# Performance work log

Measured on AMD Instinct MI355X. Metric: run time of the kernel, lower is better.

## Reference

```python
import jax, jax.numpy as jnp
import numpy as np

VEC_DIM = 128
N_DOCS = 100000
N_WORDS = 100000
B = 16384
CTX = 8
NS = 16


def setup_inputs() -> dict:
    key = jax.random.key(0)
    k1, k2, k3, k4, k5 = jax.random.split(key, 5)
    doc_ids = jax.random.randint(k1, (B,), 0, N_DOCS)
    context_ids = jax.random.randint(k2, (B, CTX), 0, N_WORDS)
    sample_ids = jax.random.randint(k3, (B, NS), 0, N_WORDS)
    paragraph_matrix = jax.random.normal(k4, (N_DOCS, VEC_DIM), dtype=jnp.float32)
    word_matrix = jax.random.normal(k5, (N_WORDS, VEC_DIM), dtype=jnp.float32)
    outputs = jnp.zeros((VEC_DIM, N_WORDS), dtype=jnp.float32)
    return {
        "doc_ids": doc_ids,
        "context_ids": context_ids,
        "sample_ids": sample_ids,
        "paragraph_matrix": paragraph_matrix,
        "word_matrix": word_matrix,
        "outputs": outputs,
    }


def reference(doc_ids, context_ids, sample_ids, paragraph_matrix, word_matrix, outputs):
    # inputs: [B, D] = doc embedding + sum of context word embeddings
    inputs = paragraph_matrix[doc_ids] + jnp.sum(word_matrix[context_ids], axis=1)
    # sampled output columns: [B, D, NS]
    out_cols = outputs[:, sample_ids].transpose(1, 0, 2)
    # batched dot products: [B, NS]
    return jnp.einsum("bd,bds->bs", inputs, out_cols)
```

## Files before the change

kernel.cpp:

```cpp
#include <hip/hip_runtime.h>

#define VEC_D   128
#define N_WORDS 100000
#define BATCH   16384
#define CTX     8
#define NS      16

__global__ __launch_bounds__(256) void transpose_kernel(
    const float* __restrict__ src,
    float* __restrict__ dst)
{
    __shared__ float lds[32][VEC_D + 1];
    const int tid = threadIdx.x;
    const int w0  = blockIdx.x * 32;

    #pragma unroll
    for (int p = 0; p < 16; ++p) {
        const int d = p * 8 + (tid >> 5);
        const int w = tid & 31;
        lds[w][d] = src[(size_t)d * N_WORDS + w0 + w];
    }
    __syncthreads();

    #pragma unroll
    for (int p = 0; p < 4; ++p) {
        const int wl = p * 8 + (tid >> 5);
        const int d4 = (tid & 31) * 4;
        float4 v = make_float4(lds[wl][d4], lds[wl][d4 + 1],
                               lds[wl][d4 + 2], lds[wl][d4 + 3]);
        *(float4*)&dst[(size_t)(w0 + wl) * VEC_D + d4] = v;
    }
}

template <bool TRANSPOSED>
__global__ __launch_bounds__(256) void dm_kernel(
    const int*   __restrict__ doc_ids,
    const int*   __restrict__ context_ids,
    const int*   __restrict__ sample_ids,
    const float* __restrict__ pm,
    const float* __restrict__ wm,
    const float* __restrict__ outsrc,
    float*       __restrict__ out)
{
    const int tid  = threadIdx.x;
    const int wave = tid >> 6;
    const int lane = tid & 63;
    const int half = lane >> 5;
    const int l    = lane & 31;
    const int b    = blockIdx.x * 8 + wave * 2 + half;
    const int d0   = l * 4;

    const int doc = doc_ids[b];
    float4 v = *(const float4*)&pm[(size_t)doc * VEC_D + d0];
    #pragma unroll
    for (int c = 0; c < CTX; ++c) {
        const int wid = context_ids[b * CTX + c];
        const float4 w4 = *(const float4*)&wm[(size_t)wid * VEC_D + d0];
        v.x += w4.x; v.y += w4.y; v.z += w4.z; v.w += w4.w;
    }

    float res = 0.0f;
    #pragma unroll
    for (int s = 0; s < NS; ++s) {
        const int wid = sample_ids[b * NS + s];
        float acc;
        if (TRANSPOSED) {
            const float4 o4 = *(const float4*)&outsrc[(size_t)wid * VEC_D + d0];
            acc = v.x * o4.x + v.y * o4.y + v.z * o4.z + v.w * o4.w;
        } else {
            acc = v.x * outsrc[(size_t)(d0 + 0) * N_WORDS + wid]
                + v.y * outsrc[(size_t)(d0 + 1) * N_WORDS + wid]
                + v.z * outsrc[(size_t)(d0 + 2) * N_WORDS + wid]
                + v.w * outsrc[(size_t)(d0 + 3) * N_WORDS + wid];
        }
        #pragma unroll
        for (int off = 16; off; off >>= 1)
            acc += __shfl_xor(acc, off, 64);
        if (l == s) res = acc;
    }
    if (l < NS)
        out[(size_t)b * NS + l] = res;
}

extern "C" void kernel_launch(void* const* d_in, const int* in_sizes, int n_in,
                              void* d_out, int out_size, void* d_ws, size_t ws_size,
                              hipStream_t stream) {
    const int*   doc_ids     = (const int*)d_in[0];
    const int*   context_ids = (const int*)d_in[1];
    const int*   sample_ids  = (const int*)d_in[2];
    const float* pm          = (const float*)d_in[3];
    const float* wm          = (const float*)d_in[4];
    const float* outputs     = (const float*)d_in[5];
    float*       out         = (float*)d_out;

    const size_t transposed_bytes = (size_t)N_WORDS * VEC_D * sizeof(float);

    if (ws_size >= transposed_bytes) {
        float* outT = (float*)d_ws;
        transpose_kernel<<<N_WORDS / 32, 256, 0, stream>>>(outputs, outT);
        dm_kernel<true><<<BATCH / 8, 256, 0, stream>>>(
            doc_ids, context_ids, sample_ids, pm, wm, outT, out);
    } else {
        dm_kernel<false><<<BATCH / 8, 256, 0, stream>>>(
            doc_ids, context_ids, sample_ids, pm, wm, outputs, out);
    }
}
```

Measured before the change: 49.68 us.

## Use 16 lanes per row with transpose-reduce and vectorized nontemporal transpose loads

Result: slower. 53.78 us (+8.3%).

```diff
diff --git a/kernel.cpp b/kernel.cpp
--- a/kernel.cpp
+++ b/kernel.cpp
@@ -5,6 +5,8 @@
 #define BATCH   16384
 #define CTX     8
 #define NS      16
+
+typedef float f32x4 __attribute__((ext_vector_type(4)));
 
 __global__ __launch_bounds__(256) void transpose_kernel(
     const float* __restrict__ src,
@@ -15,10 +17,15 @@
     const int w0  = blockIdx.x * 32;
 
     #pragma unroll
-    for (int p = 0; p < 16; ++p) {
-        const int d = p * 8 + (tid >> 5);
-        const int w = tid & 31;
-        lds[w][d] = src[(size_t)d * N_WORDS + w0 + w];
+    for (int p = 0; p < 4; ++p) {
+        const int d = p * 32 + (tid >> 3);
+        const int w = (tid & 7) * 4;
+        const f32x4 v = __builtin_nontemporal_load(
+            (const f32x4*)&src[(size_t)d * N_WORDS + w0 + w]);
+        lds[w + 0][d] = v.x;
+        lds[w + 1][d] = v.y;
+        lds[w + 2][d] = v.z;
+        lds[w + 3][d] = v.w;
     }
     __syncthreads();
 
@@ -26,9 +33,12 @@
     for (int p = 0; p < 4; ++p) {
         const int wl = p * 8 + (tid >> 5);
         const int d4 = (tid & 31) * 4;
-        float4 v = make_float4(lds[wl][d4], lds[wl][d4 + 1],
-                               lds[wl][d4 + 2], lds[wl][d4 + 3]);
-        *(float4*)&dst[(size_t)(w0 + wl) * VEC_D + d4] = v;
+        f32x4 v;
+        v.x = lds[wl][d4 + 0];
+        v.y = lds[wl][d4 + 1];
+        v.z = lds[wl][d4 + 2];
+        v.w = lds[wl][d4 + 3];
+        *(f32x4*)&dst[(size_t)(w0 + wl) * VEC_D + d4] = v;
     }
 }
 
@@ -42,44 +52,57 @@
     const float* __restrict__ outsrc,
     float*       __restrict__ out)
 {
-    const int tid  = threadIdx.x;
-    const int wave = tid >> 6;
-    const int lane = tid & 63;
-    const int half = lane >> 5;
-    const int l    = lane & 31;
-    const int b    = blockIdx.x * 8 + wave * 2 + half;
-    const int d0   = l * 4;
+    const int tid = threadIdx.x;
+    const int l   = tid & 15;
+    const int b   = blockIdx.x * 16 + (tid >> 4);
+    const int d0  = l * 8;
 
     const int doc = doc_ids[b];
-    float4 v = *(const float4*)&pm[(size_t)doc * VEC_D + d0];
+    const f32x4* pr = (const f32x4*)&pm[(size_t)doc * VEC_D + d0];
+    f32x4 v0 = pr[0], v1 = pr[1];
     #pragma unroll
     for (int c = 0; c < CTX; ++c) {
         const int wid = context_ids[b * CTX + c];
-        const float4 w4 = *(const float4*)&wm[(size_t)wid * VEC_D + d0];
-        v.x += w4.x; v.y += w4.y; v.z += w4.z; v.w += w4.w;
+        const f32x4* wr = (const f32x4*)&wm[(size_t)wid * VEC_D + d0];
+        v0 += wr[0];
+        v1 += wr[1];
     }
 
-    float res = 0.0f;
+    float acc[NS];
     #pragma unroll
     for (int s = 0; s < NS; ++s) {
         const int wid = sample_ids[b * NS + s];
-        float acc;
         if (TRANSPOSED) {
-            const float4 o4 = *(const float4*)&outsrc[(size_t)wid * VEC_D + d0];
-            acc = v.x * o4.x + v.y * o4.y + v.z * o4.z + v.w * o4.w;
+            const f32x4* orow = (const f32x4*)&outsrc[(size_t)wid * VEC_D + d0];
+            const f32x4 o0 = orow[0], o1 = orow[1];
+            acc[s] = v0.x * o0.x + v0.y * o0.y + v0.z * o0.z + v0.w * o0.w
+                   + v1.x * o1.x + v1.y * o1.y + v1.z * o1.z + v1.w * o1.w;
         } else {
-            acc = v.x * outsrc[(size_t)(d0 + 0) * N_WORDS + wid]
-                + v.y * outsrc[(size_t)(d0 + 1) * N_WORDS + wid]
-                + v.z * outsrc[(size_t)(d0 + 2) * N_WORDS + wid]
-                + v.w * outsrc[(size_t)(d0 + 3) * N_WORDS + wid];
+            float a = 0.0f;
+            #pragma unroll
+            for (int k = 0; k < 4; ++k)
+                a += v0[k] * outsrc[(size_t)(d0 + k) * N_WORDS + wid];
+            #pragma unroll
+            for (int k = 0; k < 4; ++k)
+                a += v1[k] * outsrc[(size_t)(d0 + 4 + k) * N_WORDS + wid];
+            acc[s] = a;
         }
+    }
+
+    #pragma unroll
+    for (int j = 0; j < 4; ++j) {
+        const int m = 1 << j;
+        const int h = 8 >> j;
+        const bool hi = (l & m) != 0;
         #pragma unroll
-        for (int off = 16; off; off >>= 1)
-            acc += __shfl_xor(acc, off, 64);
-        if (l == s) res = acc;
+        for (int i = 0; i < h; ++i) {
+            const float send = hi ? acc[i] : acc[h + i];
+            const float recv = __shfl_xor(send, m, 64);
+            acc[i] = (hi ? acc[h + i] : acc[i]) + recv;
+        }
     }
-    if (l < NS)
-        out[(size_t)b * NS + l] = res;
+    const int s = ((l & 1) << 3) | ((l & 2) << 1) | ((l & 4) >> 1) | ((l & 8) >> 3);
+    out[(size_t)b * NS + s] = acc[0];
 }
 
 extern "C" void kernel_launch(void* const* d_in, const int* in_sizes, int n_in,
@@ -98,10 +121,10 @@
     if (ws_size >= transposed_bytes) {
         float* outT = (float*)d_ws;
         transpose_kernel<<<N_WORDS / 32, 256, 0, stream>>>(outputs, outT);
-        dm_kernel<true><<<BATCH / 8, 256, 0, stream>>>(
+        dm_kernel<true><<<BATCH / 16, 256, 0, stream>>>(
             doc_ids, context_ids, sample_ids, pm, wm, outT, out);
     } else {
-        dm_kernel<false><<<BATCH / 8, 256, 0, stream>>>(
+        dm_kernel<false><<<BATCH / 16, 256, 0, stream>>>(
             doc_ids, context_ids, sample_ids, pm, wm, outputs, out);
     }
 }
```

## Bucket samples by output column tile instead of transposing the whole output matrix

Applied to the files above, without the earlier changes.

Result: slower. 77.00 us (+55.0%).

```diff
diff --git a/kernel.cpp b/kernel.cpp
--- a/kernel.cpp
+++ b/kernel.cpp
@@ -5,81 +5,101 @@
 #define BATCH   16384
 #define CTX     8
 #define NS      16
+#define NTILES  3125
+#define NBINS   3328
+#define CAP     256
 
-__global__ __launch_bounds__(256) void transpose_kernel(
-    const float* __restrict__ src,
-    float* __restrict__ dst)
-{
-    __shared__ float lds[32][VEC_D + 1];
-    const int tid = threadIdx.x;
-    const int w0  = blockIdx.x * 32;
+typedef float f32x4 __attribute__((ext_vector_type(4)));
+typedef int   i32x4 __attribute__((ext_vector_type(4)));
 
-    #pragma unroll
-    for (int p = 0; p < 16; ++p) {
-        const int d = p * 8 + (tid >> 5);
-        const int w = tid & 31;
-        lds[w][d] = src[(size_t)d * N_WORDS + w0 + w];
-    }
-    __syncthreads();
-
-    #pragma unroll
-    for (int p = 0; p < 4; ++p) {
-        const int wl = p * 8 + (tid >> 5);
-        const int d4 = (tid & 31) * 4;
-        float4 v = make_float4(lds[wl][d4], lds[wl][d4 + 1],
-                               lds[wl][d4 + 2], lds[wl][d4 + 3]);
-        *(float4*)&dst[(size_t)(w0 + wl) * VEC_D + d4] = v;
-    }
+__global__ __launch_bounds__(256) void zero_kernel(int* __restrict__ counts) {
+    counts[blockIdx.x * 256 + threadIdx.x] = 0;
 }
 
-template <bool TRANSPOSED>
-__global__ __launch_bounds__(256) void dm_kernel(
+__global__ __launch_bounds__(256, 4) void build_inputs_kernel(
     const int*   __restrict__ doc_ids,
     const int*   __restrict__ context_ids,
     const int*   __restrict__ sample_ids,
     const float* __restrict__ pm,
     const float* __restrict__ wm,
-    const float* __restrict__ outsrc,
+    float*       __restrict__ inputs,
+    int*         __restrict__ counts,
+    int*         __restrict__ bucket)
+{
+    const int tid = threadIdx.x;
+    const int r   = tid & 31;
+    const int b   = blockIdx.x * 8 + (tid >> 5);
+    const int d0  = r * 4;
+
+    const int doc = doc_ids[b];
+    f32x4 v = *(const f32x4*)&pm[(size_t)doc * VEC_D + d0];
+
+    const i32x4* cid = (const i32x4*)&context_ids[b * CTX];
+    #pragma unroll
+    for (int g = 0; g < 2; ++g) {
+        const i32x4 c4 = cid[g];
+        f32x4 w[4];
+        #pragma unroll
+        for (int k = 0; k < 4; ++k)
+            w[k] = *(const f32x4*)&wm[(size_t)c4[k] * VEC_D + d0];
+        #pragma unroll
+        for (int k = 0; k < 4; ++k)
+            v += w[k];
+    }
+    *(f32x4*)&inputs[(size_t)b * VEC_D + d0] = v;
+
+    if (tid < 8 * NS) {
+        const int p   = blockIdx.x * (8 * NS) + tid;
+        const int w   = sample_ids[p];
+        const int bin = w >> 5;
+        const int pos = atomicAdd(&counts[bin], 1);
+        if (pos < CAP)
+            bucket[bin * CAP + pos] = (p << 5) | (w & 31);
+    }
+}
+
+__global__ __launch_bounds__(256, 4) void dot_kernel(
+    const float* __restrict__ outputs,
+    const float* __restrict__ inputs,
+    const int*   __restrict__ counts,
+    const int*   __restrict__ bucket,
     float*       __restrict__ out)
 {
-    const int tid  = threadIdx.x;
-    const int wave = tid >> 6;
-    const int lane = tid & 63;
-    const int half = lane >> 5;
-    const int l    = lane & 31;
-    const int b    = blockIdx.x * 8 + wave * 2 + half;
-    const int d0   = l * 4;
+    __shared__ float tile[32][VEC_D];
+    const int tid = threadIdx.x;
+    const int t   = blockIdx.x;
+    const int w0  = t * 32;
 
-    const int doc = doc_ids[b];
-    float4 v = *(const float4*)&pm[(size_t)doc * VEC_D + d0];
+    const int d    = tid >> 1;
+    const int half = tid & 1;
     #pragma unroll
-    for (int c = 0; c < CTX; ++c) {
-        const int wid = context_ids[b * CTX + c];
-        const float4 w4 = *(const float4*)&wm[(size_t)wid * VEC_D + d0];
-        v.x += w4.x; v.y += w4.y; v.z += w4.z; v.w += w4.w;
+    for (int k = 0; k < 4; ++k) {
+        const int wl = half * 16 + k * 4;
+        const f32x4 vv = __builtin_nontemporal_load(
+            (const f32x4*)&outputs[(size_t)d * N_WORDS + w0 + wl]);
+        tile[wl + 0][d] = vv.x;
+        tile[wl + 1][d] = vv.y;
+        tile[wl + 2][d] = vv.z;
+        tile[wl + 3][d] = vv.w;
     }
+    __syncthreads();
 
-    float res = 0.0f;
-    #pragma unroll
-    for (int s = 0; s < NS; ++s) {
-        const int wid = sample_ids[b * NS + s];
-        float acc;
-        if (TRANSPOSED) {
-            const float4 o4 = *(const float4*)&outsrc[(size_t)wid * VEC_D + d0];
-            acc = v.x * o4.x + v.y * o4.y + v.z * o4.z + v.w * o4.w;
-        } else {
-            acc = v.x * outsrc[(size_t)(d0 + 0) * N_WORDS + wid]
-                + v.y * outsrc[(size_t)(d0 + 1) * N_WORDS + wid]
-                + v.z * outsrc[(size_t)(d0 + 2) * N_WORDS + wid]
-                + v.w * outsrc[(size_t)(d0 + 3) * N_WORDS + wid];
-        }
+    const int cnt = min(counts[t], CAP);
+    const int grp = tid >> 5;
+    const int r   = tid & 31;
+    for (int i = grp; i < cnt; i += 8) {
+        const int e  = bucket[t * CAP + i];
+        const int p  = e >> 5;
+        const int wl = e & 31;
+        const f32x4 iv = *(const f32x4*)&inputs[(size_t)(p >> 4) * VEC_D + r * 4];
+        const f32x4 ov = *(const f32x4*)&tile[wl][r * 4];
+        float a = iv.x * ov.x + iv.y * ov.y + iv.z * ov.z + iv.w * ov.w;
         #pragma unroll
-        for (int off = 16; off; off >>= 1)
-            acc += __shfl_xor(acc, off, 64);
-        if (l == s) res = acc;
+        for (int m = 16; m; m >>= 1)
+            a += __shfl_xor(a, m, 64);
+        if (r == 0)
+            out[p] = a;
     }
-    if (l < NS)
-        out[(size_t)b * NS + l] = res;
 }
 
 extern "C" void kernel_launch(void* const* d_in, const int* in_sizes, int n_in,
@@ -93,15 +113,12 @@
     const float* outputs     = (const float*)d_in[5];
     float*       out         = (float*)d_out;
 
-    const size_t transposed_bytes = (size_t)N_WORDS * VEC_D * sizeof(float);
+    float* inputs = (float*)d_ws;
+    int*   counts = (int*)((char*)d_ws + (size_t)BATCH * VEC_D * sizeof(float));
+    int*   bucket = counts + NBINS;
 
-    if (ws_size >= transposed_bytes) {
-        float* outT = (float*)d_ws;
-        transpose_kernel<<<N_WORDS / 32, 256, 0, stream>>>(outputs, outT);
-        dm_kernel<true><<<BATCH / 8, 256, 0, stream>>>(
-            doc_ids, context_ids, sample_ids, pm, wm, outT, out);
-    } else {
-        dm_kernel<false><<<BATCH / 8, 256, 0, stream>>>(
-            doc_ids, context_ids, sample_ids, pm, wm, outputs, out);
-    }
+    zero_kernel<<<NBINS / 256, 256, 0, stream>>>(counts);
+    build_inputs_kernel<<<BATCH / 8, 256, 0, stream>>>(
+        doc_ids, context_ids, sample_ids, pm, wm, inputs, counts, bucket);
+    dot_kernel<<<NTILES, 256, 0, stream>>>(outputs, inputs, counts, bucket, out);
 }
```
